# Kernel optimization log

Hardware: AMD Instinct MI355X
Metric: run time of the kernel (lower is better)

Reference implementation:

```python
import jax, jax.numpy as jnp
import numpy as np

EPS = 1e-10

def _feature_map(x):
    # fm(None) defaults to elu(x) + 1 (canonical linear-attention feature map)
    return jax.nn.elu(x) + 1.0

def setup_inputs() -> dict:
    key = jax.random.key(0)
    k1, k2, k3 = jax.random.split(key, 3)
    N, L, H, D = 4, 8192, 16, 64
    return {
        "queries": jax.random.normal(k1, (N, L, H, D), dtype=jnp.float32),
        "keys": jax.random.normal(k2, (N, L, H, D), dtype=jnp.float32),
        "values": jax.random.normal(k3, (N, L, H, D), dtype=jnp.float32),
    }

def reference(queries, keys, values):
    Q = _feature_map(queries)  # [n,l,h,d]
    K = _feature_map(keys)     # [n,s,h,d]
    # KV reduction over sequence: [n,h,m,d]
    KV = jnp.einsum('nshd,nshm->nhmd', K, values)
    # Normalizer: 1 / (Q . sum_s K) + eps (eps added AFTER reciprocal, as in source)
    Z = 1.0 / jnp.einsum('nlhd,nhd->nlh', Q, K.sum(axis=1)) + EPS
    # Output: [n,l,h,m]
    out = jnp.einsum('nlhd,nhmd,nlh->nlhm', Q, KV, Z)
    return out
```

## Files before the change

kernel.cpp:

```cpp
#include <hip/hip_runtime.h>


#define EPSV      1e-10f
#define L_SEQ     8192
#define H_HEADS   16
#define D_DIM     64
#define NH_TOT    64
#define ROWSTRIDE 1024
#define KV_STRIDE 4160
#define QSTRIDE   68

__device__ __forceinline__ float fm(float x) {
    return x > 0.0f ? x + 1.0f : __expf(x);
}

__global__ __launch_bounds__(256) void kv_reduce_kernel(
    const float* __restrict__ K, const float* __restrict__ V,
    float* __restrict__ KVg)
{
    const int t     = threadIdx.x;
    const int nh    = blockIdx.x;
    const int chunk = blockIdx.y;
    const int n  = nh >> 4, h = nh & 15;

    const int rg = t >> 4;
    const int dq = (t & 15) << 2;
    const int d0 = (t >> 4) << 2;
    const int m0 = (t & 15) << 2;

    __shared__ float Kl[32 * 64];
    __shared__ float Vl[32 * 64];
    __shared__ float ksp[16 * 64];

    float acc[4][4] = {};
    float ks[4] = {0.f, 0.f, 0.f, 0.f};

    const int base = n * (L_SEQ * ROWSTRIDE) + h * D_DIM;
    int s0 = chunk * 512;

    for (int tile = 0; tile < 16; ++tile, s0 += 32) {
#pragma unroll
        for (int p = 0; p < 2; ++p) {
            const int rr = p * 16 + rg;
            const int ga = base + (s0 + rr) * ROWSTRIDE + dq;
            const float4 kg = *reinterpret_cast<const float4*>(K + ga);
            const float4 vg = *reinterpret_cast<const float4*>(V + ga);
            float4 kf;
            kf.x = fm(kg.x); kf.y = fm(kg.y); kf.z = fm(kg.z); kf.w = fm(kg.w);
            ks[0] += kf.x; ks[1] += kf.y; ks[2] += kf.z; ks[3] += kf.w;
            *reinterpret_cast<float4*>(&Kl[rr * 64 + dq]) = kf;
            *reinterpret_cast<float4*>(&Vl[rr * 64 + dq]) = vg;
        }
        __syncthreads();
#pragma unroll 8
        for (int s = 0; s < 32; ++s) {
            const float4 k4 = *reinterpret_cast<const float4*>(&Kl[s * 64 + d0]);
            const float4 v4 = *reinterpret_cast<const float4*>(&Vl[s * 64 + m0]);
            acc[0][0] += k4.x * v4.x; acc[0][1] += k4.x * v4.y; acc[0][2] += k4.x * v4.z; acc[0][3] += k4.x * v4.w;
            acc[1][0] += k4.y * v4.x; acc[1][1] += k4.y * v4.y; acc[1][2] += k4.y * v4.z; acc[1][3] += k4.y * v4.w;
            acc[2][0] += k4.z * v4.x; acc[2][1] += k4.z * v4.y; acc[2][2] += k4.z * v4.z; acc[2][3] += k4.z * v4.w;
            acc[3][0] += k4.w * v4.x; acc[3][1] += k4.w * v4.y; acc[3][2] += k4.w * v4.z; acc[3][3] += k4.w * v4.w;
        }
        __syncthreads();
    }

    *reinterpret_cast<float4*>(&ksp[rg * 64 + dq]) = *reinterpret_cast<float4*>(ks);
    __syncthreads();

    float* kvrow = KVg + nh * KV_STRIDE;
    if (t < 64) {
        float ssum = 0.f;
#pragma unroll
        for (int g = 0; g < 16; ++g) ssum += ksp[g * 64 + t];
        atomicAdd(kvrow + 4096 + t, ssum);
    }
#pragma unroll
    for (int i = 0; i < 4; ++i) {
#pragma unroll
        for (int j = 0; j < 4; ++j) {
            atomicAdd(kvrow + (d0 + i) * 64 + (m0 + j), acc[i][j]);
        }
    }
}

__global__ __launch_bounds__(256) void out_kernel(
    const float* __restrict__ Q, const float* __restrict__ KVg,
    float* __restrict__ out)
{
    const int t      = threadIdx.x;
    const int lchunk = blockIdx.x;
    const int nh     = blockIdx.y;
    const int n = nh >> 4, h = nh & 15;

    __shared__ float Ql[64 * QSTRIDE];
    __shared__ float KVl[4096];
    __shared__ float Ks[64];
    __shared__ float zl[64];

    const float* kvrow = KVg + nh * KV_STRIDE;

#pragma unroll
    for (int j = 0; j < 4; ++j) {
        reinterpret_cast<float4*>(KVl)[t + 256 * j] =
            reinterpret_cast<const float4*>(kvrow)[t + 256 * j];
    }
    if (t < 16) {
        reinterpret_cast<float4*>(Ks)[t] =
            reinterpret_cast<const float4*>(kvrow + 4096)[t];
    }
    __syncthreads();

    const int lane16 = t & 15, grp = t >> 4;
    const int dq = lane16 << 2;
    const float4 ks4 = *reinterpret_cast<const float4*>(&Ks[dq]);
    const int qbase = (n * L_SEQ + lchunk * 64) * ROWSTRIDE + h * D_DIM;
#pragma unroll
    for (int p = 0; p < 4; ++p) {
        const int rr = p * 16 + grp;
        const float4 qg = *reinterpret_cast<const float4*>(Q + qbase + rr * ROWSTRIDE + dq);
        float4 qf;
        qf.x = fm(qg.x); qf.y = fm(qg.y); qf.z = fm(qg.z); qf.w = fm(qg.w);
        *reinterpret_cast<float4*>(&Ql[rr * QSTRIDE + dq]) = qf;
        float dp = qf.x * ks4.x + qf.y * ks4.y + qf.z * ks4.z + qf.w * ks4.w;
        dp += __shfl_xor(dp, 1);
        dp += __shfl_xor(dp, 2);
        dp += __shfl_xor(dp, 4);
        dp += __shfl_xor(dp, 8);
        if (lane16 == 0) zl[rr] = 1.0f / dp + EPSV;
    }
    __syncthreads();

    const int r0 = grp << 2;
    const int c0 = lane16 << 2;
    float acc[4][4] = {};
#pragma unroll 2
    for (int d = 0; d < 64; d += 4) {
        const float4 b0 = *reinterpret_cast<const float4*>(&KVl[(d + 0) * 64 + c0]);
        const float4 b1 = *reinterpret_cast<const float4*>(&KVl[(d + 1) * 64 + c0]);
        const float4 b2 = *reinterpret_cast<const float4*>(&KVl[(d + 2) * 64 + c0]);
        const float4 b3 = *reinterpret_cast<const float4*>(&KVl[(d + 3) * 64 + c0]);
#define DO_ROW(i) do {                                                              \
        const float4 q = *reinterpret_cast<const float4*>(&Ql[(r0 + (i)) * QSTRIDE + d]); \
        acc[i][0] += q.x * b0.x + q.y * b1.x + q.z * b2.x + q.w * b3.x;             \
        acc[i][1] += q.x * b0.y + q.y * b1.y + q.z * b2.y + q.w * b3.y;             \
        acc[i][2] += q.x * b0.z + q.y * b1.z + q.z * b2.z + q.w * b3.z;             \
        acc[i][3] += q.x * b0.w + q.y * b1.w + q.z * b2.w + q.w * b3.w;             \
    } while (0)
        DO_ROW(0); DO_ROW(1); DO_ROW(2); DO_ROW(3);
#undef DO_ROW
    }

    const int obase = qbase;
#pragma unroll
    for (int i = 0; i < 4; ++i) {
        const float z = zl[r0 + i];
        float4 o;
        o.x = acc[i][0] * z; o.y = acc[i][1] * z; o.z = acc[i][2] * z; o.w = acc[i][3] * z;
        *reinterpret_cast<float4*>(out + obase + (r0 + i) * ROWSTRIDE + c0) = o;
    }
}

extern "C" void kernel_launch(void* const* d_in, const int* in_sizes, int n_in,
                              void* d_out, int out_size, void* d_ws, size_t ws_size,
                              hipStream_t stream) {
    const float* Q = (const float*)d_in[0];
    const float* K = (const float*)d_in[1];
    const float* V = (const float*)d_in[2];
    float* out = (float*)d_out;
    float* KVg = (float*)d_ws;

    hipMemsetAsync(d_ws, 0, NH_TOT * KV_STRIDE * sizeof(float), stream);
    kv_reduce_kernel<<<dim3(NH_TOT, 16), 256, 0, stream>>>(K, V, KVg);
    out_kernel<<<dim3(L_SEQ / 64, NH_TOT), 256, 0, stream>>>(Q, KVg, out);
}
```

Before: 208.3 us.

## Split KV reduction into per-chunk partials with separate reduce kernel and register prefetch

The KV reduction can now write per-chunk partial results to distinct workspace slices instead of using atomics. A separate reduce kernel sums them, which also removes the memset. The chunk count goes up to 32 when the workspace is large enough, giving more blocks in flight. The main loop also prefetches the next K/V tile into registers while computing the current tile. In exchange it adds an extra kernel launch and extra traffic to write and read the partial slices, and the atomic fallback stays in place for small workspaces.

```diff
diff --git a/kernel.cpp b/kernel.cpp
--- a/kernel.cpp
+++ b/kernel.cpp
@@ -3,11 +3,10 @@
 
 #define EPSV      1e-10f
 #define L_SEQ     8192
-#define H_HEADS   16
-#define D_DIM     64
 #define NH_TOT    64
 #define ROWSTRIDE 1024
 #define KV_STRIDE 4160
+#define SLICE     (NH_TOT * KV_STRIDE)
 #define QSTRIDE   68
 
 __device__ __forceinline__ float fm(float x) {
@@ -16,7 +15,7 @@
 
 __global__ __launch_bounds__(256) void kv_reduce_kernel(
     const float* __restrict__ K, const float* __restrict__ V,
-    float* __restrict__ KVg)
+    float* __restrict__ ws, int tiles, int mode)
 {
     const int t     = threadIdx.x;
     const int nh    = blockIdx.x;
@@ -30,28 +29,44 @@
 
     __shared__ float Kl[32 * 64];
     __shared__ float Vl[32 * 64];
-    __shared__ float ksp[16 * 64];
 
     float acc[4][4] = {};
     float ks[4] = {0.f, 0.f, 0.f, 0.f};
 
-    const int base = n * (L_SEQ * ROWSTRIDE) + h * D_DIM;
-    int s0 = chunk * 512;
-
-    for (int tile = 0; tile < 16; ++tile, s0 += 32) {
-#pragma unroll
-        for (int p = 0; p < 2; ++p) {
-            const int rr = p * 16 + rg;
-            const int ga = base + (s0 + rr) * ROWSTRIDE + dq;
-            const float4 kg = *reinterpret_cast<const float4*>(K + ga);
-            const float4 vg = *reinterpret_cast<const float4*>(V + ga);
-            float4 kf;
-            kf.x = fm(kg.x); kf.y = fm(kg.y); kf.z = fm(kg.z); kf.w = fm(kg.w);
-            ks[0] += kf.x; ks[1] += kf.y; ks[2] += kf.z; ks[3] += kf.w;
-            *reinterpret_cast<float4*>(&Kl[rr * 64 + dq]) = kf;
-            *reinterpret_cast<float4*>(&Vl[rr * 64 + dq]) = vg;
-        }
+    const int base = n * (L_SEQ * ROWSTRIDE) + h * 64;
+    const int s0   = chunk * (tiles * 32);
+
+    float4 kr0, kr1, vr0, vr1;
+    {
+        const int ga0 = base + (s0 + rg) * ROWSTRIDE + dq;
+        const int ga1 = ga0 + 16 * ROWSTRIDE;
+        kr0 = *reinterpret_cast<const float4*>(K + ga0);
+        kr1 = *reinterpret_cast<const float4*>(K + ga1);
+        vr0 = *reinterpret_cast<const float4*>(V + ga0);
+        vr1 = *reinterpret_cast<const float4*>(V + ga1);
+    }
+
+    for (int tile = 0; tile < tiles; ++tile) {
+        float4 kf0, kf1;
+        kf0.x = fm(kr0.x); kf0.y = fm(kr0.y); kf0.z = fm(kr0.z); kf0.w = fm(kr0.w);
+        kf1.x = fm(kr1.x); kf1.y = fm(kr1.y); kf1.z = fm(kr1.z); kf1.w = fm(kr1.w);
+        ks[0] += kf0.x + kf1.x; ks[1] += kf0.y + kf1.y;
+        ks[2] += kf0.z + kf1.z; ks[3] += kf0.w + kf1.w;
+        *reinterpret_cast<float4*>(&Kl[rg * 64 + dq])        = kf0;
+        *reinterpret_cast<float4*>(&Kl[(rg + 16) * 64 + dq]) = kf1;
+        *reinterpret_cast<float4*>(&Vl[rg * 64 + dq])        = vr0;
+        *reinterpret_cast<float4*>(&Vl[(rg + 16) * 64 + dq]) = vr1;
         __syncthreads();
+
+        if (tile + 1 < tiles) {
+            const int ga0 = base + (s0 + (tile + 1) * 32 + rg) * ROWSTRIDE + dq;
+            const int ga1 = ga0 + 16 * ROWSTRIDE;
+            kr0 = *reinterpret_cast<const float4*>(K + ga0);
+            kr1 = *reinterpret_cast<const float4*>(K + ga1);
+            vr0 = *reinterpret_cast<const float4*>(V + ga0);
+            vr1 = *reinterpret_cast<const float4*>(V + ga1);
+        }
+
 #pragma unroll 8
         for (int s = 0; s < 32; ++s) {
             const float4 k4 = *reinterpret_cast<const float4*>(&Kl[s * 64 + d0]);
@@ -64,23 +79,45 @@
         __syncthreads();
     }
 
+    float* ksp = Vl;
     *reinterpret_cast<float4*>(&ksp[rg * 64 + dq]) = *reinterpret_cast<float4*>(ks);
     __syncthreads();
 
-    float* kvrow = KVg + nh * KV_STRIDE;
-    if (t < 64) {
-        float ssum = 0.f;
-#pragma unroll
-        for (int g = 0; g < 16; ++g) ssum += ksp[g * 64 + t];
-        atomicAdd(kvrow + 4096 + t, ssum);
-    }
-#pragma unroll
-    for (int i = 0; i < 4; ++i) {
-#pragma unroll
-        for (int j = 0; j < 4; ++j) {
-            atomicAdd(kvrow + (d0 + i) * 64 + (m0 + j), acc[i][j]);
-        }
-    }
+    float* dst = ws + (size_t)(mode ? (chunk * NH_TOT + nh) : nh) * KV_STRIDE;
+
+    if (mode) {
+#pragma unroll
+        for (int i = 0; i < 4; ++i) {
+            float4 o; o.x = acc[i][0]; o.y = acc[i][1]; o.z = acc[i][2]; o.w = acc[i][3];
+            *reinterpret_cast<float4*>(dst + (d0 + i) * 64 + m0) = o;
+        }
+        if (t < 64) {
+            float ssum = 0.f;
+#pragma unroll
+            for (int g = 0; g < 16; ++g) ssum += ksp[g * 64 + t];
+            dst[4096 + t] = ssum;
+        }
+    } else {
+#pragma unroll
+        for (int i = 0; i < 4; ++i)
+#pragma unroll
+            for (int j = 0; j < 4; ++j)
+                atomicAdd(dst + (d0 + i) * 64 + (m0 + j), acc[i][j]);
+        if (t < 64) {
+            float ssum = 0.f;
+#pragma unroll
+            for (int g = 0; g < 16; ++g) ssum += ksp[g * 64 + t];
+            atomicAdd(dst + 4096 + t, ssum);
+        }
+    }
+}
+
+__global__ __launch_bounds__(256) void reduce_kernel(float* __restrict__ ws, int CH)
+{
+    const int idx = blockIdx.x * 256 + threadIdx.x;
+    float s = 0.f;
+    for (int c = 0; c < CH; ++c) s += ws[(size_t)c * SLICE + idx];
+    ws[idx] = s;
 }
 
 __global__ __launch_bounds__(256) void out_kernel(
@@ -97,7 +134,7 @@
     __shared__ float Ks[64];
     __shared__ float zl[64];
 
-    const float* kvrow = KVg + nh * KV_STRIDE;
+    const float* kvrow = KVg + (size_t)nh * KV_STRIDE;
 
 #pragma unroll
     for (int j = 0; j < 4; ++j) {
@@ -113,7 +150,7 @@
     const int lane16 = t & 15, grp = t >> 4;
     const int dq = lane16 << 2;
     const float4 ks4 = *reinterpret_cast<const float4*>(&Ks[dq]);
-    const int qbase = (n * L_SEQ + lchunk * 64) * ROWSTRIDE + h * D_DIM;
+    const int qbase = (n * L_SEQ + lchunk * 64) * ROWSTRIDE + h * 64;
 #pragma unroll
     for (int p = 0; p < 4; ++p) {
         const int rr = p * 16 + grp;
@@ -167,9 +204,19 @@
     const float* K = (const float*)d_in[1];
     const float* V = (const float*)d_in[2];
     float* out = (float*)d_out;
-    float* KVg = (float*)d_ws;
-
-    hipMemsetAsync(d_ws, 0, NH_TOT * KV_STRIDE * sizeof(float), stream);
-    kv_reduce_kernel<<<dim3(NH_TOT, 16), 256, 0, stream>>>(K, V, KVg);
-    out_kernel<<<dim3(L_SEQ / 64, NH_TOT), 256, 0, stream>>>(Q, KVg, out);
-}
+    float* ws  = (float*)d_ws;
+
+    const size_t per_slice = (size_t)SLICE * sizeof(float);
+    size_t max_ch = ws_size / per_slice;
+    int CH = max_ch >= 32 ? 32 : (max_ch >= 16 ? 16 : (max_ch >= 8 ? 8 : 0));
+
+    if (CH > 0) {
+        const int tiles = (L_SEQ / 32) / CH;
+        kv_reduce_kernel<<<dim3(NH_TOT, CH), 256, 0, stream>>>(K, V, ws, tiles, 1);
+        reduce_kernel<<<SLICE / 256, 256, 0, stream>>>(ws, CH);
+    } else {
+        hipMemsetAsync(d_ws, 0, per_slice, stream);
+        kv_reduce_kernel<<<dim3(NH_TOT, 16), 256, 0, stream>>>(K, V, ws, 16, 0);
+    }
+    out_kernel<<<dim3(L_SEQ / 64, NH_TOT), 256, 0, stream>>>(Q, ws, out);
+}
```

Measured after the change: 187.3 us. 1.11x faster.
